# Kernel tuning notes

Measured on AMD Instinct MI355X. Metric: run time of the kernel, lower is better.

The kernel has to match this reference:

```python
import jax, jax.numpy as jnp
import numpy as np

B, S, E, H = 16, 512, 1024, 16
DK = E // H  # 64


def setup_inputs() -> dict:
    key = jax.random.key(0)
    ks = jax.random.split(key, 14)
    s_e = 1.0 / np.sqrt(E)
    s_d = 1.0 / np.sqrt(DK)
    return {
        "inp": jax.random.normal(ks[0], (B, S, E), dtype=jnp.float32),
        # projection linears (torch Linear stored as x @ W + b with W pre-transposed)
        "Wq": jax.random.uniform(ks[1], (E, E), jnp.float32, -s_e, s_e),
        "bq": jax.random.uniform(ks[2], (E,), jnp.float32, -s_e, s_e),
        "Wk": jax.random.uniform(ks[3], (E, E), jnp.float32, -s_e, s_e),
        "bk": jax.random.uniform(ks[4], (E,), jnp.float32, -s_e, s_e),
        "Wv": jax.random.uniform(ks[5], (E, E), jnp.float32, -s_e, s_e),
        "bv": jax.random.uniform(ks[6], (E,), jnp.float32, -s_e, s_e),
        # per-head gating linears
        "Wfq": jax.random.uniform(ks[7], (DK, DK), jnp.float32, -s_d, s_d),
        "bfq": jax.random.uniform(ks[8], (DK,), jnp.float32, -s_d, s_d),
        "Wfk": jax.random.uniform(ks[9], (DK, DK), jnp.float32, -s_d, s_d),
        "bfk": jax.random.uniform(ks[10], (DK,), jnp.float32, -s_d, s_d),
        "Wfg": jax.random.uniform(ks[11], (DK, 2 * DK), jnp.float32, -s_d, s_d),
        "bfg": jax.random.uniform(ks[12], (2 * DK,), jnp.float32, -s_d, s_d),
    }


def _split_heads(x):
    # [B, S, E] -> [B, H, S, DK]
    b, s, _ = x.shape
    return x.reshape(b, s, H, DK).transpose(0, 2, 1, 3)


def reference(inp, Wq, bq, Wk, bk, Wv, bv, Wfq, bfq, Wfk, bfk, Wfg, bfg):
    q = _split_heads(inp @ Wq + bq)  # [B,H,S,DK]
    k = _split_heads(inp @ Wk + bk)
    v = _split_heads(inp @ Wv + bv)

    # gated query/key modulation
    G = (q @ Wfq + bfq) * (k @ Wfk + bfk)          # [B,H,S,DK]
    M = jax.nn.sigmoid(G @ Wfg + bfg)              # [B,H,S,2*DK]
    q = q * M[..., :DK]
    k = k * M[..., DK:]

    scores = jnp.einsum("bhqd,bhkd->bhqk", q, k) / jnp.sqrt(jnp.asarray(DK, q.dtype))
    p_attn = jax.nn.softmax(scores, axis=-1)
    x = jnp.einsum("bhqk,bhkd->bhqd", p_attn, v)   # [B,H,S,DK]
    return x.transpose(0, 2, 1, 3).reshape(inp.shape[0], -1, H * DK)
```

## Files before the change

kernel.cpp:

```cpp
#include <hip/hip_runtime.h>


typedef __bf16 bf16;
typedef __bf16 bf16x8 __attribute__((ext_vector_type(8)));
typedef __bf16 bf16x4 __attribute__((ext_vector_type(4)));
typedef float  f32x4  __attribute__((ext_vector_type(4)));

#define MFMA16(a,b,c) __builtin_amdgcn_mfma_f32_16x16x32_bf16((a),(b),(c),0,0,0)

#define GLL16(gp, lp)                                                          \
  __builtin_amdgcn_global_load_lds(                                            \
      (__attribute__((address_space(1))) void*)(void*)(gp),                    \
      (__attribute__((address_space(3))) void*)(lp), 16, 0, 0)

__global__ __launch_bounds__(256) void k_prep(const float* __restrict__ in,
                                              bf16* __restrict__ Xb,
                                              const float* __restrict__ Wq,
                                              const float* __restrict__ Wk,
                                              const float* __restrict__ Wv,
                                              bf16* __restrict__ WT) {
  __shared__ float tile[32][33];
  const int bx = blockIdx.x, t = threadIdx.x;
  if (bx < 8192) {
    int i = bx * 256 + t;
    float4 v = ((const float4*)in)[i];
    bf16x4 o;
    o[0] = (bf16)v.x; o[1] = (bf16)v.y; o[2] = (bf16)v.z; o[3] = (bf16)v.w;
    ((bf16x4*)Xb)[i] = o;
  } else {
    int r = bx - 8192;
    int mat = r >> 10; r &= 1023;
    int kb = r >> 5, nb = r & 31;
    const float* W = (mat == 0) ? Wq : ((mat == 1) ? Wk : Wv);
    bf16* O = WT + (size_t)mat * (1024 * 1024);
    const int tr = t >> 3, tc = (t & 7) * 4;
    float4 v = *(const float4*)&W[(size_t)(kb * 32 + tr) * 1024 + nb * 32 + tc];
    tile[tr][tc] = v.x; tile[tr][tc + 1] = v.y;
    tile[tr][tc + 2] = v.z; tile[tr][tc + 3] = v.w;
    __syncthreads();
    bf16x4 o;
    o[0] = (bf16)tile[tc][tr];     o[1] = (bf16)tile[tc + 1][tr];
    o[2] = (bf16)tile[tc + 2][tr]; o[3] = (bf16)tile[tc + 3][tr];
    *(bf16x4*)&O[(size_t)(nb * 32 + tr) * 1024 + kb * 32 + tc] = o;
  }
}

__global__ __launch_bounds__(512, 2) void k_proj(const bf16* __restrict__ X,
                                                 const bf16* __restrict__ WT,
                                                 const float* __restrict__ bq,
                                                 const float* __restrict__ bk,
                                                 const float* __restrict__ bv,
                                                 bf16* __restrict__ qw,
                                                 bf16* __restrict__ kw,
                                                 bf16* __restrict__ vt) {
  extern __shared__ bf16 lds[];
  bf16* As = lds;
  bf16* Bs = lds + 32768;

  const int tid = threadIdx.x;
  const int m0 = blockIdx.x * 256;
  const int by = blockIdx.y;
  const int mat = by >> 2;
  const int n0 = (by & 3) * 256;
  const bf16* Wt = WT + (size_t)mat * (1024 * 1024);
  const float* bias = (mat == 0) ? bq : ((mat == 1) ? bk : bv);

  const int l = tid & 63, wid = tid >> 6;
  const int wm = wid >> 2, wn = wid & 3;
  const int l4 = l & 15, q8 = l >> 4;
  const int col0 = (q8 * 8) ^ ((l4 & 4) << 2);
  const int aBase = (wm * 128 + l4) * 64 + col0;
  const int bBase = (wn * 64 + l4) * 64 + col0;

  const int srow = tid >> 3;
  const int scol = ((tid & 7) * 8) ^ (((tid >> 5) & 1) << 4);
  const bf16* Xs = X + (size_t)(m0 + srow) * 1024 + scol;
  const bf16* Ws = Wt + (size_t)(n0 + srow) * 1024 + scol;
  const int ldst = tid * 8;

#define STG_A(bf, kt, h)                                                       \
  do {                                                                         \
    GLL16(Xs + (size_t)(h) * 131072 + (kt) * 64,                               \
          As + (bf) * 16384 + (h) * 8192 + ldst);                              \
    GLL16(Xs + (size_t)(h) * 131072 + 65536 + (kt) * 64,                       \
          As + (bf) * 16384 + (h) * 8192 + 4096 + ldst);                       \
  } while (0)
#define STG_B(bf, kt, h)                                                       \
  do {                                                                         \
    GLL16(Ws + (size_t)(h) * 131072 + (kt) * 64,                               \
          Bs + (bf) * 16384 + (h) * 8192 + ldst);                              \
    GLL16(Ws + (size_t)(h) * 131072 + 65536 + (kt) * 64,                       \
          Bs + (bf) * 16384 + (h) * 8192 + 4096 + ldst);                       \
  } while (0)

  f32x4 acc[8][4] = {};
  bf16x8 af[4][2], bfr[4][2];

#define LDA4(bf, qm)                                                           \
  do {                                                                         \
    _Pragma("unroll") for (int m_ = 0; m_ < 4; ++m_) {                         \
      af[m_][0] =                                                              \
          *(const bf16x8*)&As[(bf) * 16384 + aBase + ((qm) * 4 + m_) * 1024];  \
      af[m_][1] = *(const bf16x8*)&As[(bf) * 16384 + aBase +                   \
                                      ((qm) * 4 + m_) * 1024 + 32];            \
    }                                                                          \
  } while (0)
#define LDB2(bf, nh)                                                           \
  do {                                                                         \
    _Pragma("unroll") for (int n_ = 0; n_ < 2; ++n_) {                         \
      bfr[(nh) * 2 + n_][0] = *(const bf16x8*)&Bs[(bf) * 16384 + bBase +       \
                                                  ((nh) * 2 + n_) * 1024];     \
      bfr[(nh) * 2 + n_][1] = *(const bf16x8*)&Bs[(bf) * 16384 + bBase +       \
                                                  ((nh) * 2 + n_) * 1024 + 32];\
    }                                                                          \
  } while (0)
#define MMQ(qm, qn)                                                            \
  do {                                                                         \
    _Pragma("unroll") for (int kk = 0; kk < 2; ++kk)                           \
    _Pragma("unroll") for (int m_ = 0; m_ < 4; ++m_)                           \
    _Pragma("unroll") for (int n_ = 0; n_ < 2; ++n_)                           \
      acc[(qm) * 4 + m_][(qn) * 2 + n_] = MFMA16(                              \
          bfr[(qn) * 2 + n_][kk], af[m_][kk], acc[(qm) * 4 + m_][(qn) * 2 + n_]);\
  } while (0)
#define PH_PRE                                                                 \
  __builtin_amdgcn_s_barrier();                                                \
  asm volatile("s_waitcnt lgkmcnt(0)" ::: "memory");                           \
  __builtin_amdgcn_s_setprio(1)
#define PH_POST                                                                \
  __builtin_amdgcn_s_setprio(0);                                               \
  __builtin_amdgcn_s_barrier()

  STG_A(0, 0, 0); STG_A(0, 0, 1);
  STG_B(0, 0, 0); STG_B(0, 0, 1);
  STG_B(1, 1, 0); STG_B(1, 1, 1);
  asm volatile("s_waitcnt vmcnt(4)" ::: "memory");
  __builtin_amdgcn_s_barrier();

#pragma unroll 1
  for (int i = 0; i < 8; ++i) {
    const int t1 = 2 * i + 1;
    const int t2 = (i < 7) ? 2 * i + 2 : 14;
    const int t3 = (i < 7) ? 2 * i + 3 : 15;
    LDA4(0, 0); LDB2(0, 0);
    STG_A(1, t1, 0);
    PH_PRE; MMQ(0, 0); PH_POST;
    LDB2(0, 1);
    STG_A(1, t1, 1);
    PH_PRE; MMQ(0, 1); PH_POST;
    LDA4(0, 1);
    STG_B(0, t2, 0);
    PH_PRE; MMQ(1, 0); PH_POST;
    STG_B(0, t2, 1);
    PH_PRE; MMQ(1, 1);
    __builtin_amdgcn_s_setprio(0);
    asm volatile("s_waitcnt vmcnt(4)" ::: "memory");
    __builtin_amdgcn_s_barrier();
    LDA4(1, 0); LDB2(1, 0);
    STG_A(0, t2, 0);
    PH_PRE; MMQ(0, 0); PH_POST;
    LDB2(1, 1);
    STG_A(0, t2, 1);
    PH_PRE; MMQ(0, 1); PH_POST;
    LDA4(1, 1);
    STG_B(1, t3, 0);
    PH_PRE; MMQ(1, 0); PH_POST;
    STG_B(1, t3, 1);
    PH_PRE; MMQ(1, 1);
    __builtin_amdgcn_s_setprio(0);
    asm volatile("s_waitcnt vmcnt(4)" ::: "memory");
    __builtin_amdgcn_s_barrier();
  }

#pragma unroll
  for (int mi = 0; mi < 8; ++mi) {
    const int m = m0 + wm * 128 + mi * 16 + l4;
    const int b_ = m >> 9, s = m & 511;
#pragma unroll
    for (int nj = 0; nj < 4; ++nj) {
      const int nb = n0 + wn * 64 + nj * 16 + q8 * 4;
      if (mat == 2) {
#pragma unroll
        for (int r = 0; r < 4; ++r) {
          const int n = nb + r, h = n >> 6, d = n & 63;
          vt[((size_t)(b_ * 16 + h) * 64 + d) * 512 + s] =
              (bf16)(acc[mi][nj][r] + bias[n]);
        }
      } else {
        const float4 bb = *(const float4*)&bias[nb];
        bf16x4 o;
        o[0] = (bf16)(acc[mi][nj][0] + bb.x);
        o[1] = (bf16)(acc[mi][nj][1] + bb.y);
        o[2] = (bf16)(acc[mi][nj][2] + bb.z);
        o[3] = (bf16)(acc[mi][nj][3] + bb.w);
        bf16* dst = (mat == 0) ? qw : kw;
        *(bf16x4*)&dst[(size_t)m * 1024 + nb] = o;
      }
    }
  }
#undef STG_A
#undef STG_B
#undef LDA4
#undef LDB2
#undef MMQ
#undef PH_PRE
#undef PH_POST
}

__global__ __launch_bounds__(256, 2) void k_gate(bf16* __restrict__ qw,
                                                 bf16* __restrict__ kw,
                                                 const float* __restrict__ Wfq,
                                                 const float* __restrict__ bfq,
                                                 const float* __restrict__ Wfk,
                                                 const float* __restrict__ bfk,
                                                 const float* __restrict__ Wfg,
                                                 const float* __restrict__ bfg) {
  __shared__ __align__(16) char smraw[56320];
  bf16* sWq = (bf16*)smraw;
  bf16* sWk = (bf16*)(smraw + 9216);
  bf16* sWg = (bf16*)(smraw + 18432);
  bf16* sG  = (bf16*)(smraw + 36864);
  float* sb = (float*)(smraw + 55296);
  bf16* Ms  = (bf16*)smraw;
  const int tid = threadIdx.x;

  for (int idx = tid; idx < 4096; idx += 256) {
    int k = idx >> 6, n = idx & 63;
    sWq[n * 72 + k] = (bf16)Wfq[k * 64 + n];
    sWk[n * 72 + k] = (bf16)Wfk[k * 64 + n];
  }
  for (int idx = tid; idx < 8192; idx += 256) {
    int k = idx >> 7, n = idx & 127;
    sWg[n * 72 + k] = (bf16)Wfg[k * 128 + n];
  }
  if (tid < 64) { sb[tid] = bfq[tid]; sb[64 + tid] = bfk[tid]; }
  if (tid < 128) sb[128 + tid] = bfg[tid];
  __syncthreads();

  const int w = tid >> 6, l = tid & 63, l4 = l & 15, q8 = l >> 4;
  const int T0 = blockIdx.x * 128;
  const int rbase = w * 32;

  bf16x8 aq[2][2], ak[2][2];
#pragma unroll
  for (int i = 0; i < 2; ++i)
#pragma unroll
    for (int kk = 0; kk < 2; ++kk) {
      size_t off = (size_t)(T0 + rbase + i * 16 + l4) * 64 + kk * 32 + q8 * 8;
      aq[i][kk] = *(const bf16x8*)&qw[off];
      ak[i][kk] = *(const bf16x8*)&kw[off];
    }

  f32x4 fqc[2][4] = {}, fkc[2][4] = {};
#pragma unroll
  for (int j = 0; j < 4; ++j) {
    bf16x8 bq0 = *(const bf16x8*)&sWq[(j * 16 + l4) * 72 + q8 * 8];
    bf16x8 bq1 = *(const bf16x8*)&sWq[(j * 16 + l4) * 72 + 32 + q8 * 8];
    bf16x8 bk0 = *(const bf16x8*)&sWk[(j * 16 + l4) * 72 + q8 * 8];
    bf16x8 bk1 = *(const bf16x8*)&sWk[(j * 16 + l4) * 72 + 32 + q8 * 8];
#pragma unroll
    for (int i = 0; i < 2; ++i) {
      fqc[i][j] = MFMA16(aq[i][0], bq0, fqc[i][j]);
      fqc[i][j] = MFMA16(aq[i][1], bq1, fqc[i][j]);
      fkc[i][j] = MFMA16(ak[i][0], bk0, fkc[i][j]);
      fkc[i][j] = MFMA16(ak[i][1], bk1, fkc[i][j]);
    }
  }

#pragma unroll
  for (int j = 0; j < 4; ++j) {
    float bqb = sb[j * 16 + l4], bkb = sb[64 + j * 16 + l4];
#pragma unroll
    for (int i = 0; i < 2; ++i)
#pragma unroll
      for (int r = 0; r < 4; ++r) {
        int row = rbase + i * 16 + q8 * 4 + r;
        float g = (fqc[i][j][r] + bqb) * (fkc[i][j][r] + bkb);
        sG[row * 72 + j * 16 + l4] = (bf16)g;
      }
  }
  __syncthreads();

  bf16x8 ag[2][2];
#pragma unroll
  for (int i = 0; i < 2; ++i)
#pragma unroll
    for (int kk = 0; kk < 2; ++kk)
      ag[i][kk] = *(const bf16x8*)&sG[(rbase + i * 16 + l4) * 72 + kk * 32 + q8 * 8];
  f32x4 mc[2][8] = {};
#pragma unroll
  for (int jj = 0; jj < 8; ++jj) {
    bf16x8 bg0 = *(const bf16x8*)&sWg[(jj * 16 + l4) * 72 + q8 * 8];
    bf16x8 bg1 = *(const bf16x8*)&sWg[(jj * 16 + l4) * 72 + 32 + q8 * 8];
#pragma unroll
    for (int i = 0; i < 2; ++i) {
      mc[i][jj] = MFMA16(ag[i][0], bg0, mc[i][jj]);
      mc[i][jj] = MFMA16(ag[i][1], bg1, mc[i][jj]);
    }
  }

  __syncthreads();
#pragma unroll
  for (int jj = 0; jj < 8; ++jj) {
    float bgb = sb[128 + jj * 16 + l4];
#pragma unroll
    for (int i = 0; i < 2; ++i)
#pragma unroll
      for (int r = 0; r < 4; ++r) {
        int row = rbase + i * 16 + q8 * 4 + r;
        float m = mc[i][jj][r] + bgb;
        Ms[row * 136 + jj * 16 + l4] = (bf16)(1.0f / (1.0f + __expf(-m)));
      }
  }
  __syncthreads();

  const float SC = 0.18033688011112042f;
  const int tl = tid >> 1, half = tid & 1;
  bf16* base = (half ? kw : qw) + (size_t)(T0 + tl) * 64;
  const float scl = half ? 1.0f : SC;
#pragma unroll
  for (int c = 0; c < 8; ++c) {
    bf16x8 v = *(const bf16x8*)&base[c * 8];
    bf16x8 m = *(const bf16x8*)&Ms[tl * 136 + half * 64 + c * 8];
    bf16x8 o;
#pragma unroll
    for (int e = 0; e < 8; ++e)
      o[e] = (bf16)((float)v[e] * (float)m[e] * scl);
    *(bf16x8*)&base[c * 8] = o;
  }
}

__global__ __launch_bounds__(256, 2) void k_attn(const bf16* __restrict__ qw,
                                                 const bf16* __restrict__ kw,
                                                 const bf16* __restrict__ vt,
                                                 float* __restrict__ out) {
  __shared__ bf16 Kt[128 * 72];
  __shared__ bf16 Vt[64 * 136];
  __shared__ bf16 Pb[4][32 * 40];
  const int tid = threadIdx.x, w = tid >> 6, l = tid & 63;
  const int l4 = l & 15, q8 = l >> 4;
  const int bx = blockIdx.x;
  const int slot = bx >> 3;
  const int qc = slot & 3;
  const int bh = (bx & 7) + 8 * (slot >> 2);
  const int b_ = bh >> 4, h = bh & 15;
  bf16* Pw = &Pb[w][0];

  bf16x8 qf[2][2];
#pragma unroll
  for (int i = 0; i < 2; ++i)
#pragma unroll
    for (int kk = 0; kk < 2; ++kk) {
      int s = qc * 128 + w * 32 + i * 16 + l4;
      qf[i][kk] = *(const bf16x8*)
          &qw[(((size_t)b_ * 512 + s) * 16 + h) * 64 + kk * 32 + q8 * 8];
    }

  f32x4 o[2][4] = {};
  float mrun[2][4], lrun[2][4];
#pragma unroll
  for (int i = 0; i < 2; ++i)
#pragma unroll
    for (int r = 0; r < 4; ++r) { mrun[i][r] = -3.0e38f; lrun[i][r] = 0.0f; }

  for (int t = 0; t < 4; ++t) {
    __syncthreads();
#pragma unroll
    for (int i = 0; i < 4; ++i) {
      int chunk = i * 256 + tid;
      {
        int key = chunk >> 3, c8 = chunk & 7;
        bf16x8 v = *(const bf16x8*)
            &kw[(((size_t)b_ * 512 + t * 128 + key) * 16 + h) * 64 + c8 * 8];
        *(bf16x8*)&Kt[key * 72 + c8 * 8] = v;
      }
      {
        int d = chunk >> 4, c16 = chunk & 15;
        bf16x8 v = *(const bf16x8*)
            &vt[((size_t)bh * 64 + d) * 512 + t * 128 + c16 * 8];
        *(bf16x8*)&Vt[d * 136 + c16 * 8] = v;
      }
    }
    __syncthreads();

    f32x4 sc[2][8];
    const f32x4 fz = {};
#pragma unroll
    for (int c = 0; c < 8; ++c) {
      bf16x8 kb0 = *(const bf16x8*)&Kt[(c * 16 + l4) * 72 + q8 * 8];
      sc[0][c] = MFMA16(qf[0][0], kb0, fz);
      sc[1][c] = MFMA16(qf[1][0], kb0, fz);
      bf16x8 kb1 = *(const bf16x8*)&Kt[(c * 16 + l4) * 72 + 32 + q8 * 8];
      sc[0][c] = MFMA16(qf[0][1], kb1, sc[0][c]);
      sc[1][c] = MFMA16(qf[1][1], kb1, sc[1][c]);
    }

#pragma unroll
    for (int i = 0; i < 2; ++i) {
      float al[4];
#pragma unroll
      for (int r = 0; r < 4; ++r) {
        float mx = sc[i][0][r];
#pragma unroll
        for (int c = 1; c < 8; ++c) mx = fmaxf(mx, sc[i][c][r]);
        mx = fmaxf(mx, __shfl_xor(mx, 1));
        mx = fmaxf(mx, __shfl_xor(mx, 2));
        mx = fmaxf(mx, __shfl_xor(mx, 4));
        mx = fmaxf(mx, __shfl_xor(mx, 8));
        float mn = fmaxf(mrun[i][r], mx);
        al[r] = exp2f(mrun[i][r] - mn);
        mrun[i][r] = mn;
        float sm = 0.0f;
#pragma unroll
        for (int c = 0; c < 8; ++c) {
          float p = exp2f(sc[i][c][r] - mn);
          sc[i][c][r] = p;
          sm += p;
        }
        sm += __shfl_xor(sm, 1); sm += __shfl_xor(sm, 2);
        sm += __shfl_xor(sm, 4); sm += __shfl_xor(sm, 8);
        lrun[i][r] = lrun[i][r] * al[r] + sm;
      }
#pragma unroll
      for (int f = 0; f < 4; ++f)
#pragma unroll
        for (int r = 0; r < 4; ++r) o[i][f][r] *= al[r];
    }

#pragma unroll
    for (int kk2 = 0; kk2 < 4; ++kk2) {
#pragma unroll
      for (int i = 0; i < 2; ++i)
#pragma unroll
        for (int cc = 0; cc < 2; ++cc) {
          int c = kk2 * 2 + cc;
#pragma unroll
          for (int r = 0; r < 4; ++r)
            Pw[(i * 16 + q8 * 4 + r) * 40 + cc * 16 + l4] = (bf16)sc[i][c][r];
        }
      bf16x8 pa0 = *(const bf16x8*)&Pw[(l4) * 40 + q8 * 8];
      bf16x8 pa1 = *(const bf16x8*)&Pw[(16 + l4) * 40 + q8 * 8];
#pragma unroll
      for (int f = 0; f < 4; ++f) {
        bf16x8 vb = *(const bf16x8*)&Vt[(f * 16 + l4) * 136 + kk2 * 32 + q8 * 8];
        o[0][f] = MFMA16(pa0, vb, o[0][f]);
        o[1][f] = MFMA16(pa1, vb, o[1][f]);
      }
    }
  }

#pragma unroll
  for (int i = 0; i < 2; ++i)
#pragma unroll
    for (int r = 0; r < 4; ++r) {
      int srow = qc * 128 + w * 32 + i * 16 + q8 * 4 + r;
      float inv = 1.0f / lrun[i][r];
#pragma unroll
      for (int f = 0; f < 4; ++f)
        out[(((size_t)b_ * 512 + srow) * 16 + h) * 64 + f * 16 + l4] =
            o[i][f][r] * inv;
    }
}

extern "C" void kernel_launch(void* const* d_in, const int* in_sizes, int n_in,
                              void* d_out, int out_size, void* d_ws,
                              size_t ws_size, hipStream_t stream) {
  (void)in_sizes; (void)n_in; (void)out_size; (void)ws_size;
  const float* inp = (const float*)d_in[0];
  const float* Wq  = (const float*)d_in[1];
  const float* bq  = (const float*)d_in[2];
  const float* Wk  = (const float*)d_in[3];
  const float* bk  = (const float*)d_in[4];
  const float* Wv  = (const float*)d_in[5];
  const float* bv  = (const float*)d_in[6];
  const float* Wfq = (const float*)d_in[7];
  const float* bfq = (const float*)d_in[8];
  const float* Wfk = (const float*)d_in[9];
  const float* bfk = (const float*)d_in[10];
  const float* Wfg = (const float*)d_in[11];
  const float* bfg = (const float*)d_in[12];
  float* out = (float*)d_out;

  static bool s_attr = false;
  if (!s_attr) {
    (void)hipFuncSetAttribute((const void*)k_proj,
                              hipFuncAttributeMaxDynamicSharedMemorySize,
                              131072);
    s_attr = true;
  }

  char* ws = (char*)d_ws;
  bf16* Xb = (bf16*)(ws);
  bf16* WT = (bf16*)(ws + 16777216);
  bf16* qw = (bf16*)(ws + 16777216 + 6291456);
  bf16* kw = qw + 8388608;
  bf16* vt = kw + 8388608;

  k_prep<<<11264, 256, 0, stream>>>(inp, Xb, Wq, Wk, Wv, WT);
  k_proj<<<dim3(32, 12), 512, 131072, stream>>>(Xb, WT, bq, bk, bv, qw, kw, vt);
  k_gate<<<1024, 256, 0, stream>>>(qw, kw, Wfq, bfq, Wfk, bfk, Wfg, bfg);
  k_attn<<<1024, 256, 0, stream>>>(qw, kw, vt, out);
}
```

Before: 263.6 us.

## Retile QKV projection to 256x192 tiles over fused N and change LDS swizzle

Treats the three projection weights as one fused 3072-wide N dimension and retiles the projection GEMM to 256x192 block tiles, giving a 32x16 grid of 512 blocks instead of 32x12 = 384. On a 256-CU part this should fill CUs more evenly across waves. It also replaces the LDS swizzle with a row-XOR pattern to reduce bank conflicts, and rebalances the staging and MFMA phases for the smaller B tile. In exchange, each wave does less MFMA work per A-fragment load, and the output epilogue now decides the matrix per column.

Measured after the change: 259.8 us. Within noise of the previous version (-1.4%).

```diff
diff --git a/kernel.cpp b/kernel.cpp
--- a/kernel.cpp
+++ b/kernel.cpp
@@ -45,82 +45,65 @@
   }
 }
 
-__global__ __launch_bounds__(512, 2) void k_proj(const bf16* __restrict__ X,
-                                                 const bf16* __restrict__ WT,
-                                                 const float* __restrict__ bq,
-                                                 const float* __restrict__ bk,
-                                                 const float* __restrict__ bv,
-                                                 bf16* __restrict__ qw,
-                                                 bf16* __restrict__ kw,
-                                                 bf16* __restrict__ vt) {
+__global__ __launch_bounds__(512) void k_proj(const bf16* __restrict__ X,
+                                              const bf16* __restrict__ WT,
+                                              const float* __restrict__ bq,
+                                              const float* __restrict__ bk,
+                                              const float* __restrict__ bv,
+                                              bf16* __restrict__ qw,
+                                              bf16* __restrict__ kw,
+                                              bf16* __restrict__ vt) {
   extern __shared__ bf16 lds[];
   bf16* As = lds;
   bf16* Bs = lds + 32768;
 
   const int tid = threadIdx.x;
   const int m0 = blockIdx.x * 256;
-  const int by = blockIdx.y;
-  const int mat = by >> 2;
-  const int n0 = (by & 3) * 256;
-  const bf16* Wt = WT + (size_t)mat * (1024 * 1024);
-  const float* bias = (mat == 0) ? bq : ((mat == 1) ? bk : bv);
+  const int n0 = blockIdx.y * 192;
 
   const int l = tid & 63, wid = tid >> 6;
   const int wm = wid >> 2, wn = wid & 3;
   const int l4 = l & 15, q8 = l >> 4;
-  const int col0 = (q8 * 8) ^ ((l4 & 4) << 2);
-  const int aBase = (wm * 128 + l4) * 64 + col0;
-  const int bBase = (wn * 64 + l4) * 64 + col0;
+  const int cs0 = (q8 ^ (l4 & 7)) * 8;
+  const int arow = (wm * 128 + l4) * 64;
+  const int brow = (wn * 48 + l4) * 64;
 
   const int srow = tid >> 3;
-  const int scol = ((tid & 7) * 8) ^ (((tid >> 5) & 1) << 4);
+  const int scol = ((tid & 7) ^ (srow & 7)) * 8;
   const bf16* Xs = X + (size_t)(m0 + srow) * 1024 + scol;
-  const bf16* Ws = Wt + (size_t)(n0 + srow) * 1024 + scol;
+  const bf16* Ws = WT + (size_t)(n0 + srow) * 1024 + scol;
   const int ldst = tid * 8;
 
-#define STG_A(bf, kt, h)                                                       \
+#define STG_AU(bf, kt, u)                                                      \
+  GLL16(Xs + (size_t)(u) * 65536 + (kt) * 64,                                  \
+        As + (bf) * 16384 + (u) * 4096 + ldst)
+#define STG_BU(bf, kt, u)                                                      \
+  GLL16(Ws + (size_t)(u) * 65536 + (kt) * 64,                                  \
+        Bs + (bf) * 12288 + (u) * 4096 + ldst)
+
+  f32x4 acc[8][3] = {};
+  bf16x8 af[4], bfr[3][2];
+
+#define LDA(bf, qm, kk)                                                        \
   do {                                                                         \
-    GLL16(Xs + (size_t)(h) * 131072 + (kt) * 64,                               \
-          As + (bf) * 16384 + (h) * 8192 + ldst);                              \
-    GLL16(Xs + (size_t)(h) * 131072 + 65536 + (kt) * 64,                       \
-          As + (bf) * 16384 + (h) * 8192 + 4096 + ldst);                       \
+    _Pragma("unroll") for (int m_ = 0; m_ < 4; ++m_)                           \
+        af[m_] = *(const bf16x8*)&As[(bf) * 16384 + arow + (qm) * 4096 +       \
+                                     m_ * 1024 + (cs0 ^ ((kk) * 32))];         \
   } while (0)
-#define STG_B(bf, kt, h)                                                       \
+#define LDB6(bf)                                                               \
   do {                                                                         \
-    GLL16(Ws + (size_t)(h) * 131072 + (kt) * 64,                               \
-          Bs + (bf) * 16384 + (h) * 8192 + ldst);                              \
-    GLL16(Ws + (size_t)(h) * 131072 + 65536 + (kt) * 64,                       \
-          Bs + (bf) * 16384 + (h) * 8192 + 4096 + ldst);                       \
-  } while (0)
-
-  f32x4 acc[8][4] = {};
-  bf16x8 af[4][2], bfr[4][2];
-
-#define LDA4(bf, qm)                                                           \
-  do {                                                                         \
-    _Pragma("unroll") for (int m_ = 0; m_ < 4; ++m_) {                         \
-      af[m_][0] =                                                              \
-          *(const bf16x8*)&As[(bf) * 16384 + aBase + ((qm) * 4 + m_) * 1024];  \
-      af[m_][1] = *(const bf16x8*)&As[(bf) * 16384 + aBase +                   \
-                                      ((qm) * 4 + m_) * 1024 + 32];            \
+    _Pragma("unroll") for (int n_ = 0; n_ < 3; ++n_) {                         \
+      bfr[n_][0] = *(const bf16x8*)&Bs[(bf) * 12288 + brow + n_ * 1024 + cs0]; \
+      bfr[n_][1] =                                                             \
+          *(const bf16x8*)&Bs[(bf) * 12288 + brow + n_ * 1024 + (cs0 ^ 32)];   \
     }                                                                          \
   } while (0)
-#define LDB2(bf, nh)                                                           \
+#define MMQ(qm, kk)                                                            \
   do {                                                                         \
-    _Pragma("unroll") for (int n_ = 0; n_ < 2; ++n_) {                         \
-      bfr[(nh) * 2 + n_][0] = *(const bf16x8*)&Bs[(bf) * 16384 + bBase +       \
-                                                  ((nh) * 2 + n_) * 1024];     \
-      bfr[(nh) * 2 + n_][1] = *(const bf16x8*)&Bs[(bf) * 16384 + bBase +       \
-                                                  ((nh) * 2 + n_) * 1024 + 32];\
-    }                                                                          \
-  } while (0)
-#define MMQ(qm, qn)                                                            \
-  do {                                                                         \
-    _Pragma("unroll") for (int kk = 0; kk < 2; ++kk)                           \
     _Pragma("unroll") for (int m_ = 0; m_ < 4; ++m_)                           \
-    _Pragma("unroll") for (int n_ = 0; n_ < 2; ++n_)                           \
-      acc[(qm) * 4 + m_][(qn) * 2 + n_] = MFMA16(                              \
-          bfr[(qn) * 2 + n_][kk], af[m_][kk], acc[(qm) * 4 + m_][(qn) * 2 + n_]);\
+    _Pragma("unroll") for (int n_ = 0; n_ < 3; ++n_)                           \
+        acc[(qm) * 4 + m_][n_] =                                               \
+            MFMA16(bfr[n_][kk], af[m_], acc[(qm) * 4 + m_][n_]);               \
   } while (0)
 #define PH_PRE                                                                 \
   __builtin_amdgcn_s_barrier();                                                \
@@ -130,10 +113,10 @@
   __builtin_amdgcn_s_setprio(0);                                               \
   __builtin_amdgcn_s_barrier()
 
-  STG_A(0, 0, 0); STG_A(0, 0, 1);
-  STG_B(0, 0, 0); STG_B(0, 0, 1);
-  STG_B(1, 1, 0); STG_B(1, 1, 1);
-  asm volatile("s_waitcnt vmcnt(4)" ::: "memory");
+  STG_AU(0, 0, 0); STG_AU(0, 0, 1); STG_AU(0, 0, 2); STG_AU(0, 0, 3);
+  STG_BU(0, 0, 0); STG_BU(0, 0, 1); STG_BU(0, 0, 2);
+  STG_BU(1, 1, 0); STG_BU(1, 1, 1); STG_BU(1, 1, 2);
+  asm volatile("s_waitcnt vmcnt(3)" ::: "memory");
   __builtin_amdgcn_s_barrier();
 
 #pragma unroll 1
@@ -141,33 +124,35 @@
     const int t1 = 2 * i + 1;
     const int t2 = (i < 7) ? 2 * i + 2 : 14;
     const int t3 = (i < 7) ? 2 * i + 3 : 15;
-    LDA4(0, 0); LDB2(0, 0);
-    STG_A(1, t1, 0);
+    LDB6(0); LDA(0, 0, 0);
+    STG_AU(1, t1, 0); STG_AU(1, t1, 1);
     PH_PRE; MMQ(0, 0); PH_POST;
-    LDB2(0, 1);
-    STG_A(1, t1, 1);
+    LDA(0, 0, 1);
+    STG_AU(1, t1, 2); STG_AU(1, t1, 3);
     PH_PRE; MMQ(0, 1); PH_POST;
-    LDA4(0, 1);
-    STG_B(0, t2, 0);
+    LDA(0, 1, 0);
+    STG_BU(0, t2, 0); STG_BU(0, t2, 1);
     PH_PRE; MMQ(1, 0); PH_POST;
-    STG_B(0, t2, 1);
+    LDA(0, 1, 1);
+    STG_BU(0, t2, 2);
     PH_PRE; MMQ(1, 1);
     __builtin_amdgcn_s_setprio(0);
-    asm volatile("s_waitcnt vmcnt(4)" ::: "memory");
+    asm volatile("s_waitcnt vmcnt(3)" ::: "memory");
     __builtin_amdgcn_s_barrier();
-    LDA4(1, 0); LDB2(1, 0);
-    STG_A(0, t2, 0);
+    LDB6(1); LDA(1, 0, 0);
+    STG_AU(0, t2, 0); STG_AU(0, t2, 1);
     PH_PRE; MMQ(0, 0); PH_POST;
-    LDB2(1, 1);
-    STG_A(0, t2, 1);
+    LDA(1, 0, 1);
+    STG_AU(0, t2, 2); STG_AU(0, t2, 3);
     PH_PRE; MMQ(0, 1); PH_POST;
-    LDA4(1, 1);
-    STG_B(1, t3, 0);
+    LDA(1, 1, 0);
+    STG_BU(1, t3, 0); STG_BU(1, t3, 1);
     PH_PRE; MMQ(1, 0); PH_POST;
-    STG_B(1, t3, 1);
+    LDA(1, 1, 1);
+    STG_BU(1, t3, 2);
     PH_PRE; MMQ(1, 1);
     __builtin_amdgcn_s_setprio(0);
-    asm volatile("s_waitcnt vmcnt(4)" ::: "memory");
+    asm volatile("s_waitcnt vmcnt(3)" ::: "memory");
     __builtin_amdgcn_s_barrier();
   }
 
@@ -176,31 +161,33 @@
     const int m = m0 + wm * 128 + mi * 16 + l4;
     const int b_ = m >> 9, s = m & 511;
 #pragma unroll
-    for (int nj = 0; nj < 4; ++nj) {
-      const int nb = n0 + wn * 64 + nj * 16 + q8 * 4;
+    for (int nj = 0; nj < 3; ++nj) {
+      const int n = n0 + wn * 48 + nj * 16 + q8 * 4;
+      const int mat = n >> 10, nn = n & 1023;
       if (mat == 2) {
+        const int h = nn >> 6, d0 = nn & 63;
 #pragma unroll
         for (int r = 0; r < 4; ++r) {
-          const int n = nb + r, h = n >> 6, d = n & 63;
-          vt[((size_t)(b_ * 16 + h) * 64 + d) * 512 + s] =
-              (bf16)(acc[mi][nj][r] + bias[n]);
+          vt[((size_t)(b_ * 16 + h) * 64 + d0 + r) * 512 + s] =
+              (bf16)(acc[mi][nj][r] + bv[nn + r]);
         }
       } else {
-        const float4 bb = *(const float4*)&bias[nb];
+        const float* bias = (mat == 0) ? bq : bk;
+        const float4 bb = *(const float4*)&bias[nn];
         bf16x4 o;
         o[0] = (bf16)(acc[mi][nj][0] + bb.x);
         o[1] = (bf16)(acc[mi][nj][1] + bb.y);
         o[2] = (bf16)(acc[mi][nj][2] + bb.z);
         o[3] = (bf16)(acc[mi][nj][3] + bb.w);
         bf16* dst = (mat == 0) ? qw : kw;
-        *(bf16x4*)&dst[(size_t)m * 1024 + nb] = o;
-      }
-    }
-  }
-#undef STG_A
-#undef STG_B
-#undef LDA4
-#undef LDB2
+        *(bf16x4*)&dst[(size_t)m * 1024 + nn] = o;
+      }
+    }
+  }
+#undef STG_AU
+#undef STG_BU
+#undef LDA
+#undef LDB6
 #undef MMQ
 #undef PH_PRE
 #undef PH_POST
@@ -484,7 +471,7 @@
   if (!s_attr) {
     (void)hipFuncSetAttribute((const void*)k_proj,
                               hipFuncAttributeMaxDynamicSharedMemorySize,
-                              131072);
+                              114688);
     s_attr = true;
   }
 
@@ -496,7 +483,7 @@
   bf16* vt = kw + 8388608;
 
   k_prep<<<11264, 256, 0, stream>>>(inp, Xb, Wq, Wk, Wv, WT);
-  k_proj<<<dim3(32, 12), 512, 131072, stream>>>(Xb, WT, bq, bk, bv, qw, kw, vt);
+  k_proj<<<dim3(32, 16), 512, 114688, stream>>>(Xb, WT, bq, bk, bv, qw, kw, vt);
   k_gate<<<1024, 256, 0, stream>>>(qw, kw, Wfq, bfq, Wfk, bfk, Wfg, bfg);
   k_attn<<<1024, 256, 0, stream>>>(qw, kw, vt, out);
 }
```
